# Optimization experiments

Measured on AMD Instinct MI355X. Metric: run time of the kernel, lower is better.

The kernel has to match this reference:

```python
import jax, jax.numpy as jnp
import numpy as np

B, S, H = 2, 2048, 2048
NH, HD = 16, 128
TS = 512
RATE = 0.1          # custom_active_rate (used as the sampled mean, deterministic)
ALPHA = 0.5         # ts_ema_alpha
EPS = 1e-6
BASE = 10000.0
K_IDX = int((1.0 - RATE) * TS)   # torch.kthvalue k (1-indexed k-th smallest) = 460


def _rmsnorm(x, w):
    xf = x.astype(jnp.float32)
    var = jnp.mean(xf * xf, axis=-1, keepdims=True)
    return (xf * jax.lax.rsqrt(var + EPS)).astype(x.dtype) * w


def _rope_tables():
    inv = 1.0 / (BASE ** (np.arange(0, HD, 2, dtype=np.float32) / HD))
    t = np.arange(S, dtype=np.float32)
    freqs = np.outer(t, inv)                       # [S, HD/2]
    emb = np.concatenate([freqs, freqs], axis=-1)  # [S, HD]
    return jnp.asarray(np.cos(emb)), jnp.asarray(np.sin(emb))


def _rotate_half(x):
    x1, x2 = jnp.split(x, 2, axis=-1)
    return jnp.concatenate([-x2, x1], axis=-1)


def setup_inputs() -> dict:
    key = jax.random.key(0)
    ks = jax.random.split(key, 9)
    sc = 0.02
    return {
        'hidden_states': jax.random.normal(ks[0], (B, S, H), jnp.float32),
        'last_layer_ts_embedding': jax.random.normal(ks[1], (B, S, TS), jnp.float32),
        'Wq': jax.random.normal(ks[2], (H, H), jnp.float32) * sc,
        'Wk': jax.random.normal(ks[3], (H, H), jnp.float32) * sc,
        'Wv': jax.random.normal(ks[4], (H, H), jnp.float32) * sc,
        'Wo': jax.random.normal(ks[5], (H, H), jnp.float32) * sc,
        'Wts': jax.random.normal(ks[6], (H, TS), jnp.float32) * sc,
        'ts_norm_w': jnp.ones((TS,), jnp.float32),
        'Worig': jax.random.normal(ks[7], (TS, 3 * H), jnp.float32) * sc,
    }


def reference(hidden_states, last_layer_ts_embedding, Wq, Wk, Wv, Wo, Wts, ts_norm_w, Worig):
    # --- custom TS gating path ---
    ts = hidden_states @ Wts                                  # [B,S,TS]
    ts = (1.0 - ALPHA) * ts + ALPHA * last_layer_ts_embedding # EMA with previous layer
    ts = _rmsnorm(ts, ts_norm_w)
    # torch.kthvalue: k-th smallest along last dim, keepdim
    kth = jnp.sort(ts, axis=-1)[..., K_IDX - 1:K_IDX]          # [B,S,1]
    ts_filtered = jax.nn.relu(ts - kth)
    origin = ts_filtered @ Worig                               # [B,S,3H]
    q_add = origin[..., :H]
    k_add = origin[..., H:2 * H]
    v_add = k_add                                              # 'qkv' mode: v uses split[1]

    # --- qkv projections (llama linear, no bias) ---
    q = hidden_states @ Wq + q_add
    k = hidden_states @ Wk + k_add
    v = hidden_states @ Wv + v_add
    q = q.reshape(B, S, NH, HD).transpose(0, 2, 1, 3)          # [B,NH,S,HD]
    k = k.reshape(B, S, NH, HD).transpose(0, 2, 1, 3)
    v = v.reshape(B, S, NH, HD).transpose(0, 2, 1, 3)

    # --- rotary embedding ---
    cos, sin = _rope_tables()                                  # [S,HD]
    cos = cos[None, None]; sin = sin[None, None]
    q = q * cos + _rotate_half(q) * sin
    k = k * cos + _rotate_half(k) * sin

    # --- eager attention: QK^T, causal mask add, fp32 softmax, PV ---
    scores = jnp.einsum('bhqd,bhkd->bhqk', q, k) / jnp.sqrt(jnp.float32(HD))
    causal = jnp.tril(jnp.ones((S, S), bool))
    mask = jnp.where(causal, 0.0, -1e9).astype(scores.dtype)[None, None]
    probs = jax.nn.softmax((scores + mask).astype(jnp.float32), axis=-1).astype(q.dtype)
    attn = jnp.einsum('bhqk,bhkd->bhqd', probs, v)
    attn = attn.transpose(0, 2, 1, 3).reshape(B, S, H)
    return attn @ Wo
```

## Files before the change

kernel.cpp:

```cpp
#include <hip/hip_runtime.h>
#include <cstdint>

typedef __bf16 bf16_t;
typedef __bf16 bf16x8 __attribute__((ext_vector_type(8)));
typedef __bf16 bf16x4 __attribute__((ext_vector_type(4)));
typedef float  f32x4  __attribute__((ext_vector_type(4)));
typedef bf16x8 __attribute__((may_alias)) bf16x8a;
typedef bf16x4 __attribute__((may_alias)) bf16x4a;
typedef f32x4  __attribute__((may_alias)) f32x4a;

#define S_LEN 2048
#define HDIM  2048
#define NHEAD 16
#define HD    128
#define TSD   512
#define BROWS 4096
#define KIDX  459

__device__ __forceinline__ f32x4 mfma_bf16(bf16x8 a, bf16x8 b, f32x4 c) {
  return __builtin_amdgcn_mfma_f32_16x16x32_bf16(a, b, c, 0, 0, 0);
}

__device__ __forceinline__ void gld_lds16(const bf16_t* g, bf16_t* l) {
  __builtin_amdgcn_global_load_lds(
      (__attribute__((address_space(1))) void*)(void*)const_cast<bf16_t*>(g),
      (__attribute__((address_space(3))) void*)(void*)(l), 16, 0, 0);
}

__device__ __forceinline__ uint32_t pk2(float a, float b) {
  union { bf16_t h; uint16_t u; } ua, ub;
  ua.h = (bf16_t)a; ub.h = (bf16_t)b;
  return (uint32_t)ua.u | ((uint32_t)ub.u << 16);
}

__global__ void k_cvt(const float* __restrict__ in, bf16_t* __restrict__ out, int n) {
  int i = (blockIdx.x * 256 + threadIdx.x) * 4;
  if (i >= n) return;
  f32x4 v = *(const f32x4a*)(in + i);
  bf16x4 o = { (bf16_t)v.x, (bf16_t)v.y, (bf16_t)v.z, (bf16_t)v.w };
  *(bf16x4a*)(out + i) = o;
}

__global__ void k_transpose(const float* __restrict__ in, bf16_t* __restrict__ out,
                            int R, int C, int ldin) {
  __shared__ float tile[32][33];
  int c0 = blockIdx.x * 32, r0 = blockIdx.y * 32;
  int tx = threadIdx.x, ty = threadIdx.y;
  for (int i = ty; i < 32; i += 8)
    tile[i][tx] = in[(size_t)(r0 + i) * ldin + c0 + tx];
  __syncthreads();
  for (int i = ty; i < 32; i += 8)
    out[(size_t)(c0 + i) * R + r0 + tx] = (bf16_t)tile[tx][i];
}

__global__ void k_vtrans(const bf16_t* __restrict__ in, bf16_t* __restrict__ out) {
  __shared__ bf16_t t[64][72];
  int s0 = blockIdx.x * 64, d0 = blockIdx.y * 64, bh = blockIdx.z;
  const bf16_t* src = in + (size_t)bh * S_LEN * HD;
  bf16_t* dst = out + (size_t)bh * HD * S_LEN;
  int tid = threadIdx.x;
  for (int g = tid; g < 512; g += 256) {
    int r = g >> 3, cc = g & 7;
    *(bf16x8a*)&t[r][cc * 8] = *(const bf16x8a*)(src + (size_t)(s0 + r) * HD + d0 + cc * 8);
  }
  __syncthreads();
  for (int g = tid; g < 512; g += 256) {
    int dr = g >> 3, sc = g & 7;
    bf16x8 v;
#pragma unroll
    for (int j = 0; j < 8; j++) v[j] = t[sc * 8 + j][dr];
    *(bf16x8a*)(dst + (size_t)(d0 + dr) * S_LEN + s0 + sc * 8) = v;
  }
}

template<int MODE>
__global__ __launch_bounds__(256)
void k_gemm(const bf16_t* __restrict__ A, const bf16_t* __restrict__ Bt,
            float* __restrict__ outF, bf16_t* __restrict__ outB,
            const bf16_t* __restrict__ addend, int M, int N, int K,
            int addLd, int addCol)
{
  __shared__ __align__(16) bf16_t As[128 * 32];
  __shared__ __align__(16) bf16_t Bs[128 * 32];
  const int tid  = threadIdx.x;
  const int lane = tid & 63, w = tid >> 6;
  const int quad = lane >> 4, l15 = lane & 15;
  const int m0 = blockIdx.y * 128, n0 = blockIdx.x * 128;
  const int wm = (w >> 1) * 64, wn = (w & 1) * 64;

  f32x4 acc[4][4];
#pragma unroll
  for (int i = 0; i < 4; i++)
#pragma unroll
    for (int j = 0; j < 4; j++) { f32x4 z = {0.f,0.f,0.f,0.f}; acc[i][j] = z; }

  const int srow = w * 16 + (lane >> 2);
  const int scol = (lane & 3) * 8;

  for (int k0 = 0; k0 < K; k0 += 32) {
    __syncthreads();
    gld_lds16(A  + (size_t)(m0 +      srow) * K + k0 + scol, As + (size_t)w * 512);
    gld_lds16(A  + (size_t)(m0 + 64 + srow) * K + k0 + scol, As + (size_t)(4 + w) * 512);
    gld_lds16(Bt + (size_t)(n0 +      srow) * K + k0 + scol, Bs + (size_t)w * 512);
    gld_lds16(Bt + (size_t)(n0 + 64 + srow) * K + k0 + scol, Bs + (size_t)(4 + w) * 512);
    __syncthreads();
    bf16x8 af[4], bv[4];
#pragma unroll
    for (int i = 0; i < 4; i++)
      af[i] = *(const bf16x8a*)&As[(wm + i * 16 + l15) * 32 + quad * 8];
#pragma unroll
    for (int j = 0; j < 4; j++)
      bv[j] = *(const bf16x8a*)&Bs[(wn + j * 16 + l15) * 32 + quad * 8];
#pragma unroll
    for (int i = 0; i < 4; i++)
#pragma unroll
      for (int j = 0; j < 4; j++)
        acc[i][j] = mfma_bf16(af[i], bv[j], acc[i][j]);
  }

#pragma unroll
  for (int i = 0; i < 4; i++)
#pragma unroll
    for (int j = 0; j < 4; j++)
#pragma unroll
      for (int r = 0; r < 4; r++) {
        int row = m0 + wm + i * 16 + quad * 4 + r;
        int col = n0 + wn + j * 16 + l15;
        float v = acc[i][j][r];
        if (MODE == 0) {
          outF[(size_t)row * N + col] = v;
        } else if (MODE == 1) {
          outB[(size_t)row * N + col] = (bf16_t)v;
        } else {
          v += (float)addend[(size_t)row * addLd + addCol + col];
          int s = row & (S_LEN - 1), b = row >> 11;
          int h = col >> 7, d = col & (HD - 1);
          outB[(((size_t)(b * NHEAD + h) * S_LEN) + s) * HD + d] = (bf16_t)v;
        }
      }
}

__global__ __launch_bounds__(256)
void k_tsproc(const float* __restrict__ ts, const float* __restrict__ lte,
              const float* __restrict__ wn, bf16_t* __restrict__ tsf)
{
  __shared__ float sv[TSD];
  __shared__ float red[4];
  int row = blockIdx.x;
  int t = threadIdx.x;
  const float* tr = ts  + (size_t)row * TSD;
  const float* lr = lte + (size_t)row * TSD;
  float v0 = 0.5f * tr[t] + 0.5f * lr[t];
  float v1 = 0.5f * tr[t + 256] + 0.5f * lr[t + 256];
  float ss = v0 * v0 + v1 * v1;
#pragma unroll
  for (int o = 32; o > 0; o >>= 1) ss += __shfl_down(ss, o);
  int lane = t & 63, wv = t >> 6;
  if (lane == 0) red[wv] = ss;
  __syncthreads();
  float tot = red[0] + red[1] + red[2] + red[3];
  float scl = rsqrtf(tot * (1.0f / TSD) + 1e-6f);
  float n0 = v0 * scl * wn[t];
  float n1 = v1 * scl * wn[t + 256];
  sv[t] = n0; sv[t + 256] = n1;
  __syncthreads();
  for (int k = 2; k <= TSD; k <<= 1) {
    for (int j = k >> 1; j > 0; j >>= 1) {
#pragma unroll
      for (int u = 0; u < 2; u++) {
        int idx = t + u * 256;
        int ixj = idx ^ j;
        if (ixj > idx) {
          float a = sv[idx], b = sv[ixj];
          bool up = ((idx & k) == 0);
          if ((a > b) == up) { sv[idx] = b; sv[ixj] = a; }
        }
      }
      __syncthreads();
    }
  }
  float kth = sv[KIDX];
  tsf[(size_t)row * TSD + t]       = (bf16_t)fmaxf(n0 - kth, 0.0f);
  tsf[(size_t)row * TSD + t + 256] = (bf16_t)fmaxf(n1 - kth, 0.0f);
}

__global__ void k_ropetab(float* __restrict__ tabC, float* __restrict__ tabS) {
  int gid = blockIdx.x * 256 + threadIdx.x;
  int d = gid & 63, s = gid >> 6;
  float inv = powf(10000.0f, (float)(-2 * d) * (1.0f / 128.0f));
  float sn, c;
  sincosf((float)s * inv, &sn, &c);
  tabC[gid] = c; tabS[gid] = sn;
}

__global__ void k_rope(bf16_t* __restrict__ x, const float* __restrict__ tabC,
                       const float* __restrict__ tabS) {
  int gid = blockIdx.x * 256 + threadIdx.x;
  int d = gid & 63;
  int rowi = gid >> 6;
  int s = rowi & (S_LEN - 1);
  bf16_t* p = x + (size_t)rowi * HD;
  float c  = tabC[s * 64 + d];
  float sn = tabS[s * 64 + d];
  float x0 = (float)p[d], x1 = (float)p[d + 64];
  p[d]      = (bf16_t)(x0 * c - x1 * sn);
  p[d + 64] = (bf16_t)(x1 * c + x0 * sn);
}

__global__ __launch_bounds__(512, 4)
void k_attn(const bf16_t* __restrict__ qb, const bf16_t* __restrict__ kb,
            const bf16_t* __restrict__ vtb, bf16_t* __restrict__ attnB)
{
  __shared__ __align__(16) bf16_t Kt[2][64 * 128];
  __shared__ __align__(16) bf16_t Vt[2][128 * 64];

  const int bid = blockIdx.x;
  const int bh  = (bid & 7) + 8 * (bid >> 7);
  static const int qmap[16] = {15,0,14,1,13,2,12,3,11,4,10,5,9,6,8,7};
  const int q0 = qmap[((bid >> 3) + (bid >> 8)) & 15] * 128;

  const int tid = threadIdx.x;
  const int lane = tid & 63, w = tid >> 6;
  const int quad = lane >> 4, l15 = lane & 15;

  const bf16_t* Q  = qb  + (size_t)bh * S_LEN * HD;
  const bf16_t* Kg = kb  + (size_t)bh * S_LEN * HD;
  const bf16_t* Vg = vtb + (size_t)bh * HD * S_LEN;

  bf16x8 qf[4];
  {
    const bf16_t* qrow = Q + (size_t)(q0 + w * 16 + l15) * HD;
#pragma unroll
    for (int c = 0; c < 4; c++)
      qf[c] = *(const bf16x8a*)(qrow + c * 32 + quad * 8);
  }

  int kfo[4];
#pragma unroll
  for (int c = 0; c < 4; c++)
    kfo[c] = l15 * 128 + (((c * 4 + quad) ^ (l15 & 7)) * 8);
  int vfo[2];
#pragma unroll
  for (int kc = 0; kc < 2; kc++)
    vfo[kc] = l15 * 64 + (((kc * 4 + quad) ^ (l15 & 7)) * 8);

  const int kR   = tid >> 4;
  const int kCg  = tid & 15;
  const size_t kG = (size_t)kR * HD + kCg * 8;
  const int kL   = kR * 128 + ((kCg ^ (kR & 7)) * 8);
  const int vD0  = tid >> 3;
  const int vKg  = tid & 7;
  const size_t vG = (size_t)vD0 * S_LEN + vKg * 8;
  const int vL   = vD0 * 64 + ((vKg ^ (vD0 & 7)) * 8);

  const int addrA = 4 * (l15 + 32 * (quad & 1));
  const int addrB = addrA + 64;
  const bool selHi = (quad >> 1) != 0;

  f32x4 o[8];
#pragma unroll
  for (int t8 = 0; t8 < 8; t8++) { f32x4 z = {0.f,0.f,0.f,0.f}; o[t8] = z; }
  float m_i = -1e30f, l_i = 0.0f;

  const float scale = 0.08838834764831845f;
  const int kEnd = q0 + 64;
  const int qrow_i = q0 + w * 16 + l15;

  bf16x8 kr0, kr1, vr0, vr1;
  kr0 = *(const bf16x8a*)(Kg + kG);
  kr1 = *(const bf16x8a*)(Kg + kG + (size_t)32 * HD);
  vr0 = *(const bf16x8a*)(Vg + vG);
  vr1 = *(const bf16x8a*)(Vg + vG + (size_t)64 * S_LEN);
  *(bf16x8a*)(&Kt[0][0] + kL)        = kr0;
  *(bf16x8a*)(&Kt[0][0] + kL + 4096) = kr1;
  *(bf16x8a*)(&Vt[0][0] + vL)        = vr0;
  *(bf16x8a*)(&Vt[0][0] + vL + 4096) = vr1;
  {
    const int t1 = (64 <= kEnd) ? 64 : 0;
    kr0 = *(const bf16x8a*)(Kg + (size_t)t1 * HD + kG);
    kr1 = *(const bf16x8a*)(Kg + (size_t)t1 * HD + kG + (size_t)32 * HD);
    vr0 = *(const bf16x8a*)(Vg + vG + t1);
    vr1 = *(const bf16x8a*)(Vg + vG + t1 + (size_t)64 * S_LEN);
  }
  __syncthreads();

  int p = 0;
  for (int k0 = 0; k0 <= kEnd; k0 += 64) {
    const bf16_t* Kb = &Kt[p][0];
    const bf16_t* Vb = &Vt[p][0];

    f32x4 st_[4];
#pragma unroll
    for (int nt = 0; nt < 4; nt++) { f32x4 z = {0.f,0.f,0.f,0.f}; st_[nt] = z; }
#pragma unroll
    for (int nt = 0; nt < 4; nt++)
#pragma unroll
      for (int c = 0; c < 4; c++) {
        bf16x8 kf = *(const bf16x8a*)(Kb + kfo[c] + nt * 2048);
        st_[nt] = mfma_bf16(kf, qf[c], st_[nt]);
      }

    if (k0 + 64 <= kEnd) {
      bf16_t* Kw = &Kt[p ^ 1][0];
      bf16_t* Vw = &Vt[p ^ 1][0];
      *(bf16x8a*)(Kw + kL)        = kr0;
      *(bf16x8a*)(Kw + kL + 4096) = kr1;
      *(bf16x8a*)(Vw + vL)        = vr0;
      *(bf16x8a*)(Vw + vL + 4096) = vr1;
      const int t2 = (k0 + 128 <= kEnd) ? (k0 + 128) : kEnd;
      kr0 = *(const bf16x8a*)(Kg + (size_t)t2 * HD + kG);
      kr1 = *(const bf16x8a*)(Kg + (size_t)t2 * HD + kG + (size_t)32 * HD);
      vr0 = *(const bf16x8a*)(Vg + vG + t2);
      vr1 = *(const bf16x8a*)(Vg + vG + t2 + (size_t)64 * S_LEN);
    }

    if (k0 + 63 > q0 + w * 16) {
#pragma unroll
      for (int nt = 0; nt < 4; nt++)
#pragma unroll
        for (int r = 0; r < 4; r++) {
          int key = k0 + nt * 16 + quad * 4 + r;
          float v = st_[nt][r] * scale;
          st_[nt][r] = (key > qrow_i) ? -1e9f : v;
        }
    } else {
#pragma unroll
      for (int nt = 0; nt < 4; nt++)
#pragma unroll
        for (int r = 0; r < 4; r++)
          st_[nt][r] *= scale;
    }

    float mx = st_[0][0];
#pragma unroll
    for (int nt = 0; nt < 4; nt++)
#pragma unroll
      for (int r = 0; r < 4; r++) mx = fmaxf(mx, st_[nt][r]);
    mx = fmaxf(mx, __shfl_xor(mx, 16));
    mx = fmaxf(mx, __shfl_xor(mx, 32));
    float mnew = fmaxf(m_i, mx);
    float alpha = __expf(m_i - mnew);
    m_i = mnew;
    float rs = 0.0f;
#pragma unroll
    for (int nt = 0; nt < 4; nt++)
#pragma unroll
      for (int r = 0; r < 4; r++) {
        float pv = __expf(st_[nt][r] - mnew);
        st_[nt][r] = pv;
        rs += pv;
      }
    rs += __shfl_xor(rs, 16);
    rs += __shfl_xor(rs, 32);
    l_i = l_i * alpha + rs;

    uint32_t pk[4][2];
#pragma unroll
    for (int nt = 0; nt < 4; nt++) {
      pk[nt][0] = pk2(st_[nt][0], st_[nt][1]);
      pk[nt][1] = pk2(st_[nt][2], st_[nt][3]);
    }

#pragma unroll
    for (int t8 = 0; t8 < 8; t8++)
#pragma unroll
      for (int r = 0; r < 4; r++)
        o[t8][r] *= alpha;

#pragma unroll
    for (int kc = 0; kc < 2; kc++) {
      uint32_t a0 = __builtin_amdgcn_ds_bpermute(addrA, (int)pk[2*kc][0]);
      uint32_t a1 = __builtin_amdgcn_ds_bpermute(addrA, (int)pk[2*kc][1]);
      uint32_t a2 = __builtin_amdgcn_ds_bpermute(addrB, (int)pk[2*kc][0]);
      uint32_t a3 = __builtin_amdgcn_ds_bpermute(addrB, (int)pk[2*kc][1]);
      uint32_t b0 = __builtin_amdgcn_ds_bpermute(addrA, (int)pk[2*kc+1][0]);
      uint32_t b1 = __builtin_amdgcn_ds_bpermute(addrA, (int)pk[2*kc+1][1]);
      uint32_t b2 = __builtin_amdgcn_ds_bpermute(addrB, (int)pk[2*kc+1][0]);
      uint32_t b3 = __builtin_amdgcn_ds_bpermute(addrB, (int)pk[2*kc+1][1]);
      union { bf16x8 v; uint32_t d[4]; } pf;
      pf.d[0] = selHi ? b0 : a0;
      pf.d[1] = selHi ? b1 : a1;
      pf.d[2] = selHi ? b2 : a2;
      pf.d[3] = selHi ? b3 : a3;
#pragma unroll
      for (int t8 = 0; t8 < 8; t8++) {
        bf16x8 vf = *(const bf16x8a*)(Vb + vfo[kc] + t8 * 1024);
        o[t8] = mfma_bf16(vf, pf.v, o[t8]);
      }
    }

    __syncthreads();
    p ^= 1;
  }

  const int b = bh >> 4, h = bh & 15;
  const float rl = 1.0f / l_i;
  uint32_t* outp = (uint32_t*)(attnB + (size_t)(b * S_LEN + qrow_i) * HDIM + h * HD);
#pragma unroll
  for (int t8 = 0; t8 < 8; t8++)
#pragma unroll
    for (int pr = 0; pr < 2; pr++) {
      uint32_t v = pk2(o[t8][2*pr] * rl, o[t8][2*pr+1] * rl);
      outp[t8 * 8 + quad * 2 + pr] = v;
    }
}

extern "C" void kernel_launch(void* const* d_in, const int* in_sizes, int n_in,
                              void* d_out, int out_size, void* d_ws, size_t ws_size,
                              hipStream_t stream) {
  const float* hs    = (const float*)d_in[0];
  const float* lte   = (const float*)d_in[1];
  const float* Wq    = (const float*)d_in[2];
  const float* Wk    = (const float*)d_in[3];
  const float* Wv    = (const float*)d_in[4];
  const float* Wo    = (const float*)d_in[5];
  const float* Wts   = (const float*)d_in[6];
  const float* tsw   = (const float*)d_in[7];
  const float* Worig = (const float*)d_in[8];
  float* out = (float*)d_out;

  char* p = (char*)d_ws;
  bf16_t* hsB   = (bf16_t*)(p);
  bf16_t* wT    = (bf16_t*)(p + 16777216);
  float*  tsB   = (float*)(p + 25165824);
  bf16_t* tsf   = (bf16_t*)(p + 33554432);
  bf16_t* qkadd = (bf16_t*)(p + 37748736);
  bf16_t* attnB = qkadd;
  bf16_t* vtb   = (bf16_t*)(p + 54525952);
  bf16_t* qbuf  = (bf16_t*)(p + 71303168);
  bf16_t* kbuf  = (bf16_t*)(p + 88080384);
  bf16_t* vbuf  = (bf16_t*)(p + 104857600);
  float*  tabC  = tsB;
  float*  tabS  = tsB + 131072;

  k_cvt<<<8192, 256, 0, stream>>>(hs, hsB, BROWS * HDIM);
  k_transpose<<<dim3(16, 64), dim3(32, 8), 0, stream>>>(Wts, wT, 2048, 512, 512);
  k_gemm<0><<<dim3(4, 32), 256, 0, stream>>>(hsB, wT, tsB, nullptr, nullptr,
                                             4096, 512, 2048, 0, 0);
  k_tsproc<<<4096, 256, 0, stream>>>(tsB, lte, tsw, tsf);
  k_ropetab<<<512, 256, 0, stream>>>(tabC, tabS);
  k_transpose<<<dim3(128, 16), dim3(32, 8), 0, stream>>>(Worig, wT, 512, 4096, 6144);
  k_gemm<1><<<dim3(32, 32), 256, 0, stream>>>(tsf, wT, nullptr, qkadd, nullptr,
                                              4096, 4096, 512, 0, 0);
  k_transpose<<<dim3(64, 64), dim3(32, 8), 0, stream>>>(Wq, wT, 2048, 2048, 2048);
  k_gemm<2><<<dim3(16, 32), 256, 0, stream>>>(hsB, wT, nullptr, qbuf, qkadd,
                                              4096, 2048, 2048, 4096, 0);
  k_transpose<<<dim3(64, 64), dim3(32, 8), 0, stream>>>(Wk, wT, 2048, 2048, 2048);
  k_gemm<2><<<dim3(16, 32), 256, 0, stream>>>(hsB, wT, nullptr, kbuf, qkadd,
                                              4096, 2048, 2048, 4096, 2048);
  k_transpose<<<dim3(64, 64), dim3(32, 8), 0, stream>>>(Wv, wT, 2048, 2048, 2048);
  k_gemm<2><<<dim3(16, 32), 256, 0, stream>>>(hsB, wT, nullptr, vbuf, qkadd,
                                              4096, 2048, 2048, 4096, 2048);
  k_rope<<<16384, 256, 0, stream>>>(qbuf, tabC, tabS);
  k_rope<<<16384, 256, 0, stream>>>(kbuf, tabC, tabS);
  k_vtrans<<<dim3(32, 2, 32), 256, 0, stream>>>(vbuf, vtb);
  k_transpose<<<dim3(64, 64), dim3(32, 8), 0, stream>>>(Wo, wT, 2048, 2048, 2048);
  k_attn<<<512, 512, 0, stream>>>(qbuf, kbuf, vtb, attnB);
  k_gemm<0><<<dim3(16, 32), 256, 0, stream>>>(attnB, wT, out, nullptr, nullptr,
                                              4096, 2048, 2048, 0, 0);
}
```

Before: 636.1 us.

## Shrink attention blocks to 64 query rows with single-buffered LDS and lazy rescale

Attention blocks shrink from 512 to 256 threads with 64 query rows each, doubling the grid and halving the number of K tiles wasted on the diagonal. LDS drops from double to single buffering, with global prefetch into registers, to raise occupancy. Running-max rescaling of the output accumulator is skipped unless the max grows by more than a threshold, and s_setprio is placed around the MFMA loops. The aim is less work on masked tiles, more concurrent blocks and fewer VALU rescales, at the cost of an extra barrier stall each iteration and some numeric risk from the deferred max update.

```diff
diff --git a/kernel.cpp b/kernel.cpp
--- a/kernel.cpp
+++ b/kernel.cpp
@@ -207,17 +207,18 @@
   p[d + 64] = (bf16_t)(x1 * c + x0 * sn);
 }
 
-__global__ __launch_bounds__(512, 4)
+__global__ __launch_bounds__(256, 4)
 void k_attn(const bf16_t* __restrict__ qb, const bf16_t* __restrict__ kb,
             const bf16_t* __restrict__ vtb, bf16_t* __restrict__ attnB)
 {
-  __shared__ __align__(16) bf16_t Kt[2][64 * 128];
-  __shared__ __align__(16) bf16_t Vt[2][128 * 64];
+  __shared__ __align__(16) bf16_t Kt[64 * 128];
+  __shared__ __align__(16) bf16_t Vt[128 * 64];
 
   const int bid = blockIdx.x;
-  const int bh  = (bid & 7) + 8 * (bid >> 7);
-  static const int qmap[16] = {15,0,14,1,13,2,12,3,11,4,10,5,9,6,8,7};
-  const int q0 = qmap[((bid >> 3) + (bid >> 8)) & 15] * 128;
+  const int bh  = (bid & 7) + 8 * (bid >> 8);
+  static const int qmap[32] = {31,0,30,1,29,2,28,3,27,4,26,5,25,6,24,7,
+                               23,8,22,9,21,10,20,11,19,12,18,13,17,14,16,15};
+  const int q0 = qmap[((bid >> 3) + (bid >> 8)) & 31] * 64;
 
   const int tid = threadIdx.x;
   const int lane = tid & 63, w = tid >> 6;
@@ -244,14 +245,17 @@
   for (int kc = 0; kc < 2; kc++)
     vfo[kc] = l15 * 64 + (((kc * 4 + quad) ^ (l15 & 7)) * 8);
 
-  const int kR   = tid >> 4;
-  const int kCg  = tid & 15;
-  const size_t kG = (size_t)kR * HD + kCg * 8;
-  const int kL   = kR * 128 + ((kCg ^ (kR & 7)) * 8);
-  const int vD0  = tid >> 3;
-  const int vKg  = tid & 7;
-  const size_t vG = (size_t)vD0 * S_LEN + vKg * 8;
-  const int vL   = vD0 * 64 + ((vKg ^ (vD0 & 7)) * 8);
+  int kGo[4], kLo[4], vGo[4], vLo[4];
+#pragma unroll
+  for (int j = 0; j < 4; j++) {
+    int g  = tid + 256 * j;
+    int kR = g >> 4, kC = g & 15;
+    kGo[j] = kR * HD + kC * 8;
+    kLo[j] = kR * 128 + ((kC ^ (kR & 7)) * 8);
+    int vD = g >> 3, vK = g & 7;
+    vGo[j] = vD * S_LEN + vK * 8;
+    vLo[j] = vD * 64 + ((vK ^ (vD & 7)) * 8);
+  }
 
   const int addrA = 4 * (l15 + 32 * (quad & 1));
   const int addrB = addrA + 64;
@@ -263,58 +267,47 @@
   float m_i = -1e30f, l_i = 0.0f;
 
   const float scale = 0.08838834764831845f;
-  const int kEnd = q0 + 64;
+  const int kEnd = q0;
   const int qrow_i = q0 + w * 16 + l15;
 
-  bf16x8 kr0, kr1, vr0, vr1;
-  kr0 = *(const bf16x8a*)(Kg + kG);
-  kr1 = *(const bf16x8a*)(Kg + kG + (size_t)32 * HD);
-  vr0 = *(const bf16x8a*)(Vg + vG);
-  vr1 = *(const bf16x8a*)(Vg + vG + (size_t)64 * S_LEN);
-  *(bf16x8a*)(&Kt[0][0] + kL)        = kr0;
-  *(bf16x8a*)(&Kt[0][0] + kL + 4096) = kr1;
-  *(bf16x8a*)(&Vt[0][0] + vL)        = vr0;
-  *(bf16x8a*)(&Vt[0][0] + vL + 4096) = vr1;
-  {
-    const int t1 = (64 <= kEnd) ? 64 : 0;
-    kr0 = *(const bf16x8a*)(Kg + (size_t)t1 * HD + kG);
-    kr1 = *(const bf16x8a*)(Kg + (size_t)t1 * HD + kG + (size_t)32 * HD);
-    vr0 = *(const bf16x8a*)(Vg + vG + t1);
-    vr1 = *(const bf16x8a*)(Vg + vG + t1 + (size_t)64 * S_LEN);
-  }
-  __syncthreads();
-
-  int p = 0;
+  bf16x8 kr[4], vr[4];
+#pragma unroll
+  for (int j = 0; j < 4; j++) {
+    kr[j] = *(const bf16x8a*)(Kg + kGo[j]);
+    vr[j] = *(const bf16x8a*)(Vg + vGo[j]);
+  }
+
   for (int k0 = 0; k0 <= kEnd; k0 += 64) {
-    const bf16_t* Kb = &Kt[p][0];
-    const bf16_t* Vb = &Vt[p][0];
+#pragma unroll
+    for (int j = 0; j < 4; j++) {
+      *(bf16x8a*)(Kt + kLo[j]) = kr[j];
+      *(bf16x8a*)(Vt + vLo[j]) = vr[j];
+    }
+    if (k0 < kEnd) {
+      const bf16_t* Kn = Kg + (size_t)(k0 + 64) * HD;
+      const bf16_t* Vn = Vg + (k0 + 64);
+#pragma unroll
+      for (int j = 0; j < 4; j++) {
+        kr[j] = *(const bf16x8a*)(Kn + kGo[j]);
+        vr[j] = *(const bf16x8a*)(Vn + vGo[j]);
+      }
+    }
+    __syncthreads();
 
     f32x4 st_[4];
 #pragma unroll
     for (int nt = 0; nt < 4; nt++) { f32x4 z = {0.f,0.f,0.f,0.f}; st_[nt] = z; }
+    __builtin_amdgcn_s_setprio(1);
 #pragma unroll
     for (int nt = 0; nt < 4; nt++)
 #pragma unroll
       for (int c = 0; c < 4; c++) {
-        bf16x8 kf = *(const bf16x8a*)(Kb + kfo[c] + nt * 2048);
+        bf16x8 kf = *(const bf16x8a*)(Kt + kfo[c] + nt * 2048);
         st_[nt] = mfma_bf16(kf, qf[c], st_[nt]);
       }
-
-    if (k0 + 64 <= kEnd) {
-      bf16_t* Kw = &Kt[p ^ 1][0];
-      bf16_t* Vw = &Vt[p ^ 1][0];
-      *(bf16x8a*)(Kw + kL)        = kr0;
-      *(bf16x8a*)(Kw + kL + 4096) = kr1;
-      *(bf16x8a*)(Vw + vL)        = vr0;
-      *(bf16x8a*)(Vw + vL + 4096) = vr1;
-      const int t2 = (k0 + 128 <= kEnd) ? (k0 + 128) : kEnd;
-      kr0 = *(const bf16x8a*)(Kg + (size_t)t2 * HD + kG);
-      kr1 = *(const bf16x8a*)(Kg + (size_t)t2 * HD + kG + (size_t)32 * HD);
-      vr0 = *(const bf16x8a*)(Vg + vG + t2);
-      vr1 = *(const bf16x8a*)(Vg + vG + t2 + (size_t)64 * S_LEN);
-    }
-
-    if (k0 + 63 > q0 + w * 16) {
+    __builtin_amdgcn_s_setprio(0);
+
+    if (k0 == q0) {
 #pragma unroll
       for (int nt = 0; nt < 4; nt++)
 #pragma unroll
@@ -338,21 +331,31 @@
       for (int r = 0; r < 4; r++) mx = fmaxf(mx, st_[nt][r]);
     mx = fmaxf(mx, __shfl_xor(mx, 16));
     mx = fmaxf(mx, __shfl_xor(mx, 32));
-    float mnew = fmaxf(m_i, mx);
-    float alpha = __expf(m_i - mnew);
-    m_i = mnew;
+
+    if (__ballot(mx > m_i + 8.0f)) {
+      float mnew = fmaxf(m_i, mx);
+      float alpha = __expf(m_i - mnew);
+      m_i = mnew;
+      l_i *= alpha;
+#pragma unroll
+      for (int t8 = 0; t8 < 8; t8++)
+#pragma unroll
+        for (int r = 0; r < 4; r++)
+          o[t8][r] *= alpha;
+    }
+
     float rs = 0.0f;
 #pragma unroll
     for (int nt = 0; nt < 4; nt++)
 #pragma unroll
       for (int r = 0; r < 4; r++) {
-        float pv = __expf(st_[nt][r] - mnew);
+        float pv = __expf(st_[nt][r] - m_i);
         st_[nt][r] = pv;
         rs += pv;
       }
     rs += __shfl_xor(rs, 16);
     rs += __shfl_xor(rs, 32);
-    l_i = l_i * alpha + rs;
+    l_i += rs;
 
     uint32_t pk[4][2];
 #pragma unroll
@@ -360,12 +363,6 @@
       pk[nt][0] = pk2(st_[nt][0], st_[nt][1]);
       pk[nt][1] = pk2(st_[nt][2], st_[nt][3]);
     }
-
-#pragma unroll
-    for (int t8 = 0; t8 < 8; t8++)
-#pragma unroll
-      for (int r = 0; r < 4; r++)
-        o[t8][r] *= alpha;
 
 #pragma unroll
     for (int kc = 0; kc < 2; kc++) {
@@ -382,15 +379,16 @@
       pf.d[1] = selHi ? b1 : a1;
       pf.d[2] = selHi ? b2 : a2;
       pf.d[3] = selHi ? b3 : a3;
+      __builtin_amdgcn_s_setprio(1);
 #pragma unroll
       for (int t8 = 0; t8 < 8; t8++) {
-        bf16x8 vf = *(const bf16x8a*)(Vb + vfo[kc] + t8 * 1024);
+        bf16x8 vf = *(const bf16x8a*)(Vt + vfo[kc] + t8 * 1024);
         o[t8] = mfma_bf16(vf, pf.v, o[t8]);
       }
+      __builtin_amdgcn_s_setprio(0);
     }
 
     __syncthreads();
-    p ^= 1;
   }
 
   const int b = bh >> 4, h = bh & 15;
@@ -455,7 +453,7 @@
   k_rope<<<16384, 256, 0, stream>>>(kbuf, tabC, tabS);
   k_vtrans<<<dim3(32, 2, 32), 256, 0, stream>>>(vbuf, vtb);
   k_transpose<<<dim3(64, 64), dim3(32, 8), 0, stream>>>(Wo, wT, 2048, 2048, 2048);
-  k_attn<<<512, 512, 0, stream>>>(qbuf, kbuf, vtb, attnB);
+  k_attn<<<1024, 256, 0, stream>>>(qbuf, kbuf, vtb, attnB);
   k_gemm<0><<<dim3(16, 32), 256, 0, stream>>>(attnB, wT, out, nullptr, nullptr,
                                               4096, 2048, 2048, 0, 0);
 }
```

After: 690.2 us. 1.08x slower.
